# Kernel optimization log

Measured on AMD Instinct MI355X. Metric: run time of the kernel, lower is better.

The kernel has to match this reference:

```python
import jax, jax.numpy as jnp
import numpy as np

DIM = 512
HEADS = 8
HD = DIM // HEADS

def _rotate_half(t):
    t1, t2 = jnp.split(t, 2, axis=-1)
    return jnp.concatenate((-t2, t1), axis=-1)

def _layernorm(x, g, b, eps=1e-5):
    mu = jnp.mean(x, axis=-1, keepdims=True)
    var = jnp.var(x, axis=-1, keepdims=True)
    return (x - mu) * jax.lax.rsqrt(var + eps) * g + b

def setup_inputs() -> dict:
    key = jax.random.key(0)
    ks = jax.random.split(key, 12)
    B, S = 4, 2048
    x = jax.random.normal(ks[0], (B, S, DIM), dtype=jnp.float32)
    rope_cos = jax.random.uniform(ks[1], (1, S, 1, HD), dtype=jnp.float32)
    rope_sin = jax.random.uniform(ks[2], (1, S, 1, HD), dtype=jnp.float32)
    sd = 1.0 / np.sqrt(DIM)
    params = {
        'norm1_g': jnp.ones((DIM,), jnp.float32),
        'norm1_b': jnp.zeros((DIM,), jnp.float32),
        'norm2_g': jnp.ones((DIM,), jnp.float32),
        'norm2_b': jnp.zeros((DIM,), jnp.float32),
        'w_qkv': jax.random.uniform(ks[3], (DIM, 3 * DIM), jnp.float32, -sd, sd),
        'b_qkv': jax.random.uniform(ks[4], (3 * DIM,), jnp.float32, -sd, sd),
        'w_proj': jax.random.uniform(ks[5], (DIM, DIM), jnp.float32, -sd, sd),
        'b_proj': jax.random.uniform(ks[6], (DIM,), jnp.float32, -sd, sd),
        'w_fc1': jax.random.uniform(ks[7], (DIM, 4 * DIM), jnp.float32, -sd, sd),
        'b_fc1': jax.random.uniform(ks[8], (4 * DIM,), jnp.float32, -sd, sd),
        'w_fc2': jax.random.uniform(ks[9], (4 * DIM, DIM), jnp.float32, -1.0 / np.sqrt(4 * DIM), 1.0 / np.sqrt(4 * DIM)),
        'b_fc2': jax.random.uniform(ks[10], (DIM,), jnp.float32, -1.0 / np.sqrt(4 * DIM), 1.0 / np.sqrt(4 * DIM)),
    }
    return {'x': x, 'rope_cos': rope_cos, 'rope_sin': rope_sin, **params}

def reference(x, rope_cos, rope_sin, norm1_g, norm1_b, norm2_g, norm2_b,
              w_qkv, b_qkv, w_proj, b_proj, w_fc1, b_fc1, w_fc2, b_fc2):
    B, S, D = x.shape
    scale = 1.0 / np.sqrt(HD)
    shortcut = x
    h = _layernorm(x, norm1_g, norm1_b)
    qkv = (h @ w_qkv + b_qkv).reshape(B, S, 3, HEADS, HD)
    q, k, v = qkv[:, :, 0], qkv[:, :, 1], qkv[:, :, 2]  # [B,S,H,hd]
    q = q * rope_cos + _rotate_half(q) * rope_sin
    k = k * rope_cos + _rotate_half(k) * rope_sin
    # attention over heads: scores [B,H,S,S]
    attn = jnp.einsum('bqhd,bkhd->bhqk', q, k) * scale
    attn = jax.nn.softmax(attn, axis=-1)
    o = jnp.einsum('bhqk,bkhd->bqhd', attn, v).reshape(B, S, D)
    o = o @ w_proj + b_proj
    x = shortcut + o  # dropout is identity in eval
    h2 = _layernorm(x, norm2_g, norm2_b)
    mlp = jax.nn.gelu(h2 @ w_fc1 + b_fc1, approximate=False) @ w_fc2 + b_fc2
    return x + mlp
```

## Files before the change

### kernel.cpp

```cpp
#include <hip/hip_runtime.h>
#include <cstdint>
#include <cstddef>

typedef unsigned short u16;
typedef unsigned int   u32;
typedef __bf16 bf16x8 __attribute__((ext_vector_type(8)));
typedef float  f32x4  __attribute__((ext_vector_type(4)));

#define BS   8192
#define DIMM 512
#define NH   8
#define HD   64
#define SEQ  2048
#define DFF  2048
#define NQKV 1536

#define GLD16(g, l) __builtin_amdgcn_global_load_lds( \
    (__attribute__((address_space(1))) const void*)(g), \
    (__attribute__((address_space(3))) void*)(l), 16, 0, 0)

__device__ __forceinline__ float b2f(u16 s) {
  u32 u = ((u32)s) << 16;
  float f; __builtin_memcpy(&f, &u, 4); return f;
}
__device__ __forceinline__ u16 f2b(float f) {
  u32 u; __builtin_memcpy(&u, &f, 4);
  u += 0x7fffu + ((u >> 16) & 1u);
  return (u16)(u >> 16);
}
__device__ __forceinline__ u16 f2b_rtz(float f) {
  u32 u; __builtin_memcpy(&u, &f, 4);
  return (u16)(u >> 16);
}

#define SZ_QKV (DIMM * NQKV)
#define SZ_PRJ (DIMM * DIMM)
#define SZ_F1  (DIMM * DFF)
#define SZ_F2  (DFF * DIMM)
__global__ __launch_bounds__(256) void transpose_all_k(
    const float* __restrict__ w_qkv, const float* __restrict__ w_prj,
    const float* __restrict__ w_f1,  const float* __restrict__ w_f2,
    u16* __restrict__ o_qkv, u16* __restrict__ o_prj,
    u16* __restrict__ o_f1,  u16* __restrict__ o_f2) {
  int idx = blockIdx.x * 256 + threadIdx.x;
  const float* W; u16* O; int Kd, Nd, off;
  if (idx < SZ_QKV)                         { W = w_qkv; O = o_qkv; Kd = DIMM; Nd = NQKV; off = idx; }
  else if (idx < SZ_QKV + SZ_PRJ)           { W = w_prj; O = o_prj; Kd = DIMM; Nd = DIMM; off = idx - SZ_QKV; }
  else if (idx < SZ_QKV + SZ_PRJ + SZ_F1)   { W = w_f1;  O = o_f1;  Kd = DIMM; Nd = DFF;  off = idx - SZ_QKV - SZ_PRJ; }
  else                                      { W = w_f2;  O = o_f2;  Kd = DFF;  Nd = DIMM; off = idx - SZ_QKV - SZ_PRJ - SZ_F1; }
  int n = off / Kd, k = off - n * Kd;
  O[off] = f2b(W[(size_t)k * Nd + n]);
}

__global__ __launch_bounds__(256) void ln_f32b_k(const float* __restrict__ X,
    const float* __restrict__ G, const float* __restrict__ Bb, u16* __restrict__ out) {
  int w = threadIdx.x >> 6, lane = threadIdx.x & 63;
  size_t row = (size_t)blockIdx.x * 4 + w;
  const float* xr = X + row * DIMM;
  float v[8];
  *(float4*)&v[0] = *(const float4*)(xr + lane * 8);
  *(float4*)&v[4] = *(const float4*)(xr + lane * 8 + 4);
  float s = 0.f, s2 = 0.f;
#pragma unroll
  for (int j = 0; j < 8; j++) { s += v[j]; s2 += v[j] * v[j]; }
#pragma unroll
  for (int m = 1; m < 64; m <<= 1) { s += __shfl_xor(s, m); s2 += __shfl_xor(s2, m); }
  float mu = s * (1.f / DIMM);
  float rsd = rsqrtf(s2 * (1.f / DIMM) - mu * mu + 1e-5f);
  float g[8], bb[8];
  *(float4*)&g[0]  = *(const float4*)(G + lane * 8);
  *(float4*)&g[4]  = *(const float4*)(G + lane * 8 + 4);
  *(float4*)&bb[0] = *(const float4*)(Bb + lane * 8);
  *(float4*)&bb[4] = *(const float4*)(Bb + lane * 8 + 4);
  uint4 ov; u16* os = (u16*)&ov;
#pragma unroll
  for (int j = 0; j < 8; j++) os[j] = f2b((v[j] - mu) * rsd * g[j] + bb[j]);
  *(uint4*)(out + row * DIMM + lane * 8) = ov;
}

template <int EPI, int TM>
__global__ __launch_bounds__(256) void gemm_bt(const u16* __restrict__ A,
    const u16* __restrict__ BT, const float* __restrict__ bias,
    void* __restrict__ Cout, const float* __restrict__ resid, int N, int Kd) {
  __shared__ u16 a_s[TM * 32];
  __shared__ u16 b_s[128 * 32];
  int t = threadIdx.x, lane = t & 63, w = t >> 6;
  int l15 = lane & 15, quad = lane >> 4;
  int gx = gridDim.x;
  int lid = blockIdx.x + gx * blockIdx.y;
  int per = (gx * gridDim.y) >> 3;
  int nid = (lid & 7) * per + (lid >> 3);
  int bx = nid % gx, by = nid / gx;
  int m0 = by * TM, n0 = bx * 128;
  constexpr int MT = TM / 32;
  int wm = (w >> 1) * (TM / 2), wn = (w & 1) * 64;
  f32x4 z4 = {0.f, 0.f, 0.f, 0.f};
  f32x4 acc[MT][4];
#pragma unroll
  for (int i = 0; i < MT; i++)
#pragma unroll
    for (int j = 0; j < 4; j++) acc[i][j] = z4;

  for (int k0 = 0; k0 < Kd; k0 += 32) {
    __syncthreads();
#pragma unroll
    for (int i = 0; i < TM / 64; i++) {
      int c = t + i * 256;
      int row = c >> 2, ch = c & 3;
      GLD16(A + (size_t)(m0 + row) * Kd + k0 + ch * 8, &a_s[c * 8]);
    }
#pragma unroll
    for (int i = 0; i < 2; i++) {
      int c = t + i * 256;
      int row = c >> 2, ch = c & 3;
      GLD16(BT + (size_t)(n0 + row) * Kd + k0 + ch * 8, &b_s[c * 8]);
    }
    __syncthreads();
    bf16x8 af[MT], bfm[4];
#pragma unroll
    for (int mt = 0; mt < MT; mt++) af[mt] = *(const bf16x8*)&a_s[(wm + mt * 16 + l15) * 32 + quad * 8];
#pragma unroll
    for (int nt = 0; nt < 4; nt++) bfm[nt] = *(const bf16x8*)&b_s[(wn + nt * 16 + l15) * 32 + quad * 8];
#pragma unroll
    for (int mt = 0; mt < MT; mt++)
#pragma unroll
      for (int nt = 0; nt < 4; nt++)
        acc[mt][nt] = __builtin_amdgcn_mfma_f32_16x16x32_bf16(af[mt], bfm[nt], acc[mt][nt], 0, 0, 0);
  }

#pragma unroll
  for (int nt = 0; nt < 4; nt++) {
    int col = n0 + wn + nt * 16 + l15;
    float bv = bias[col];
#pragma unroll
    for (int mt = 0; mt < MT; mt++) {
#pragma unroll
      for (int r = 0; r < 4; r++) {
        int rw = m0 + wm + mt * 16 + quad * 4 + r;
        float v = acc[mt][nt][r] + bv;
        size_t off = (size_t)rw * N + col;
        if (EPI == 0) {
          ((float*)Cout)[off] = v;
        } else if (EPI == 1) {
          ((float*)Cout)[off] = v + resid[off];
        } else if (EPI == 2) {
          ((u16*)Cout)[off] = f2b(0.5f * v * (1.f + erff(v * 0.70710678118654752f)));
        } else {
          ((u16*)Cout)[off] = f2b(v);
        }
      }
    }
  }
}

#define QSCALE 0.18033688f
__global__ __launch_bounds__(256) void rope_k(const u16* __restrict__ qkv,
    const float* __restrict__ C, const float* __restrict__ Sn,
    u16* __restrict__ Qo, u16* __restrict__ Ko, u16* __restrict__ Vo) {
  int idx = blockIdx.x * 256 + threadIdx.x;
  int row = idx / 192;
  int cn = idx - row * 192;
  int n0 = cn * 8;
  int comp = n0 >> 9;
  int hh = (n0 >> 6) & 7;
  int d0 = n0 & 63;
  int b = row >> 11, s = row & 2047;
  const u16* src = qkv + (size_t)row * NQKV;
  uint4 val = *(const uint4*)(src + n0);
  u16* vs = (u16*)&val;
  size_t oo = ((size_t)((b << 3) + hh) * SEQ + s) * HD + d0;
  if (comp == 2) { *(uint4*)(Vo + oo) = val; return; }
  uint4 pv = *(const uint4*)(src + (n0 ^ 32));
  u16* ps = (u16*)&pv;
  float cv[8], sv[8];
  *(float4*)&cv[0] = *(const float4*)(C + s * HD + d0);
  *(float4*)&cv[4] = *(const float4*)(C + s * HD + d0 + 4);
  *(float4*)&sv[0] = *(const float4*)(Sn + s * HD + d0);
  *(float4*)&sv[4] = *(const float4*)(Sn + s * HD + d0 + 4);
  float sgn = (d0 & 32) ? 1.f : -1.f;
  float sc = (comp == 0) ? QSCALE : 1.f;
  uint4 ov; u16* os = (u16*)&ov;
#pragma unroll
  for (int j = 0; j < 8; j++)
    os[j] = f2b(sc * (b2f(vs[j]) * cv[j] + sgn * b2f(ps[j]) * sv[j]));
  *(uint4*)((comp == 0 ? Qo : Ko) + oo) = ov;
}

__global__ __launch_bounds__(512) void attn_flash_k(const u16* __restrict__ Qg,
    const u16* __restrict__ Kg, const u16* __restrict__ Vg, u16* __restrict__ Og) {
  __shared__ u16 q_s[128 * 72];
  __shared__ u16 k_s[64 * 72];
  __shared__ u16 vt_s[64 * 72];
  int t = threadIdx.x, lane = t & 63, w = t >> 6;
  int l15 = lane & 15, quad = lane >> 4;
  int lid = blockIdx.x;
  int nid = (lid & 7) * 64 + (lid >> 3);
  int bh = nid >> 4;
  int qt0 = (nid & 15) * 128;
  int b = bh >> 3, h = bh & 7;
  const u16* Qp = Qg + (size_t)bh * SEQ * HD;
  const u16* Kp = Kg + (size_t)bh * SEQ * HD;
  const u16* Vp = Vg + (size_t)bh * SEQ * HD;
  int row = t >> 3, ch = t & 7;
  int r8 = row >> 3, r0 = row & 7;

#pragma unroll
  for (int i = 0; i < 2; i++) {
    int c = t + i * 512, qr = c >> 3, qc = c & 7;
    *(uint4*)&q_s[qr * 72 + qc * 8] = *(const uint4*)(Qp + (size_t)(qt0 + qr) * HD + qc * 8);
  }
  uint4 kr = *(const uint4*)(Kp + (size_t)row * HD + ch * 8);
  uint4 vr = *(const uint4*)(Vp + (size_t)row * HD + ch * 8);
  __syncthreads();
  bf16x8 qa[2];
  qa[0] = *(const bf16x8*)&q_s[(w * 16 + l15) * 72 + quad * 8];
  qa[1] = *(const bf16x8*)&q_s[(w * 16 + l15) * 72 + 32 + quad * 8];
  u16* p_s = q_s;
  f32x4 z4 = {0.f, 0.f, 0.f, 0.f};
  f32x4 of[4];
#pragma unroll
  for (int n = 0; n < 4; n++) of[n] = z4;
  float lrun[4] = {};

  for (int kt = 0; kt < SEQ; kt += 64) {
    __syncthreads();
    *(uint4*)&k_s[row * 72 + ch * 8] = kr;
    {
      u16* v0 = (u16*)&vr;
#pragma unroll
      for (int j = 0; j < 8; j++) {
        int d = ch * 8 + j;
        vt_s[d * 72 + ((r8 ^ ch) << 3) + r0] = v0[j];
      }
    }
    __syncthreads();
    if (kt + 64 < SEQ) {
      kr = *(const uint4*)(Kp + (size_t)(kt + 64 + row) * HD + ch * 8);
      vr = *(const uint4*)(Vp + (size_t)(kt + 64 + row) * HD + ch * 8);
    }
    f32x4 sf[4];
#pragma unroll
    for (int n = 0; n < 4; n++) sf[n] = z4;
    __builtin_amdgcn_s_setprio(1);
#pragma unroll
    for (int kk = 0; kk < 2; kk++)
#pragma unroll
      for (int n = 0; n < 4; n++) {
        bf16x8 kb = *(const bf16x8*)&k_s[(n * 16 + l15) * 72 + kk * 32 + quad * 8];
        sf[n] = __builtin_amdgcn_mfma_f32_16x16x32_bf16(qa[kk], kb, sf[n], 0, 0, 0);
      }
    __builtin_amdgcn_s_setprio(0);
#pragma unroll
    for (int r = 0; r < 4; r++) {
      int prow = (w * 16 + quad * 4 + r) * 72;
#pragma unroll
      for (int n = 0; n < 4; n++) {
        float pp = exp2f(sf[n][r]);
        lrun[r] += pp;
        p_s[prow + n * 16 + l15] = f2b_rtz(pp);
      }
    }
    __builtin_amdgcn_s_setprio(1);
#pragma unroll
    for (int kk = 0; kk < 2; kk++) {
      bf16x8 pa = *(const bf16x8*)&p_s[(w * 16 + l15) * 72 + kk * 32 + quad * 8];
#pragma unroll
      for (int n = 0; n < 4; n++) {
        bf16x8 vb = *(const bf16x8*)&vt_s[(n * 16 + l15) * 72 +
                     (((kk * 4 + quad) ^ (2 * n + (l15 >> 3))) << 3)];
        of[n] = __builtin_amdgcn_mfma_f32_16x16x32_bf16(pa, vb, of[n], 0, 0, 0);
      }
    }
    __builtin_amdgcn_s_setprio(0);
  }
#pragma unroll
  for (int r = 0; r < 4; r++) {
    float l = lrun[r];
#pragma unroll
    for (int m = 1; m < 16; m <<= 1) l += __shfl_xor(l, m);
    float inv = 1.f / l;
    size_t orow = (size_t)(b * SEQ + qt0 + w * 16 + quad * 4 + r);
#pragma unroll
    for (int n = 0; n < 4; n++)
      Og[orow * DIMM + h * HD + n * 16 + l15] = f2b(of[n][r] * inv);
  }
}

extern "C" void kernel_launch(void* const* d_in, const int* in_sizes, int n_in,
                              void* d_out, int out_size, void* d_ws, size_t ws_size,
                              hipStream_t stream) {
  const float* x    = (const float*)d_in[0];
  const float* rc   = (const float*)d_in[1];
  const float* rsn  = (const float*)d_in[2];
  const float* n1g  = (const float*)d_in[3];
  const float* n1b  = (const float*)d_in[4];
  const float* n2g  = (const float*)d_in[5];
  const float* n2b  = (const float*)d_in[6];
  const float* wqkv = (const float*)d_in[7];
  const float* bqkv = (const float*)d_in[8];
  const float* wprj = (const float*)d_in[9];
  const float* bprj = (const float*)d_in[10];
  const float* wf1  = (const float*)d_in[11];
  const float* bf1  = (const float*)d_in[12];
  const float* wf2  = (const float*)d_in[13];
  const float* bf2  = (const float*)d_in[14];

  char* p = (char*)d_ws;
  u16*   wqkvT = (u16*)p;
  u16*   wprjT = (u16*)(p + (2u  << 20));
  u16*   wf1T  = (u16*)(p + (3u  << 20));
  u16*   wf2T  = (u16*)(p + (5u  << 20));
  u16*   h1    = (u16*)(p + (8u  << 20));
  u16*   qkvb  = (u16*)(p + (16u << 20));
  u16*   Qb    = (u16*)(p + (64u << 20));
  u16*   Kb    = (u16*)(p + (72u << 20));
  u16*   Vb    = (u16*)(p + (80u << 20));
  float* x2    = (float*)(p + (88u << 20));
  u16*   ob    = h1;
  u16*   h2    = h1;
  u16*   mid   = qkvb;

  transpose_all_k<<<dim3((SZ_QKV + SZ_PRJ + SZ_F1 + SZ_F2) / 256), 256, 0, stream>>>(
      wqkv, wprj, wf1, wf2, wqkvT, wprjT, wf1T, wf2T);

  ln_f32b_k<<<dim3(BS / 4), 256, 0, stream>>>(x, n1g, n1b, h1);

  gemm_bt<3, 128><<<dim3(NQKV / 128, BS / 128), 256, 0, stream>>>(h1, wqkvT, bqkv, qkvb, nullptr, NQKV, DIMM);

  rope_k<<<dim3(BS * NQKV / 8 / 256), 256, 0, stream>>>(qkvb, rc, rsn, Qb, Kb, Vb);

  attn_flash_k<<<dim3(32 * (SEQ / 128)), 512, 0, stream>>>(Qb, Kb, Vb, ob);

  gemm_bt<1, 64><<<dim3(DIMM / 128, BS / 64), 256, 0, stream>>>(ob, wprjT, bprj, x2, x, DIMM, DIMM);

  ln_f32b_k<<<dim3(BS / 4), 256, 0, stream>>>(x2, n2g, n2b, h2);

  gemm_bt<2, 128><<<dim3(DFF / 128, BS / 128), 256, 0, stream>>>(h2, wf1T, bf1, mid, nullptr, DFF, DIMM);

  gemm_bt<1, 64><<<dim3(DIMM / 128, BS / 64), 256, 0, stream>>>(mid, wf2T, bf2, (float*)d_out, x2, DIMM, DFF);
}
```

Measured before the change: 312.5 us.

## Double-buffer GEMM LDS tiles with XOR swizzle and retile N=512 GEMMs

The GEMM kernel now uses two LDS buffers, so the async global-to-LDS loads for the next K step are issued while MFMAs run on the current one. This halves the barriers per K step. LDS chunks are XOR-swizzled to cut bank conflicts on fragment reads. The projection and FC2 GEMMs move to 64x64 tiles with BK=64, where each wave owns a 16-row strip, which doubles block count for those narrow-N launches. The cost is double the LDS use, and the loop assumes an even number of K steps.

```diff
diff --git a/kernel.cpp b/kernel.cpp
--- a/kernel.cpp
+++ b/kernel.cpp
@@ -78,12 +78,20 @@
   *(uint4*)(out + row * DIMM + lane * 8) = ov;
 }
 
-template <int EPI, int TM>
+template <int EPI, int TM, int TN, int BK>
 __global__ __launch_bounds__(256) void gemm_bt(const u16* __restrict__ A,
     const u16* __restrict__ BT, const float* __restrict__ bias,
     void* __restrict__ Cout, const float* __restrict__ resid, int N, int Kd) {
-  __shared__ u16 a_s[TM * 32];
-  __shared__ u16 b_s[128 * 32];
+  constexpr int CPR  = BK / 8;
+  constexpr int CPRB = (BK == 64) ? 3 : 2;
+  constexpr int RS   = (BK == 64) ? 0 : 1;
+  constexpr int KK   = BK / 32;
+  constexpr int WROWS = (TN == 128) ? TM / 2 : TM / 4;
+  constexpr int MT   = WROWS / 16;
+  constexpr int ALOOP = TM * CPR / 256;
+  constexpr int BLOOP = TN * CPR / 256;
+  __shared__ __align__(16) u16 a_s[2][TM * BK];
+  __shared__ __align__(16) u16 b_s[2][TN * BK];
   int t = threadIdx.x, lane = t & 63, w = t >> 6;
   int l15 = lane & 15, quad = lane >> 4;
   int gx = gridDim.x;
@@ -91,9 +99,9 @@
   int per = (gx * gridDim.y) >> 3;
   int nid = (lid & 7) * per + (lid >> 3);
   int bx = nid % gx, by = nid / gx;
-  int m0 = by * TM, n0 = bx * 128;
-  constexpr int MT = TM / 32;
-  int wm = (w >> 1) * (TM / 2), wn = (w & 1) * 64;
+  int m0 = by * TM, n0 = bx * TN;
+  int wm = (TN == 128) ? (w >> 1) * WROWS : w * WROWS;
+  int wn = (TN == 128) ? (w & 1) * 64 : 0;
   f32x4 z4 = {0.f, 0.f, 0.f, 0.f};
   f32x4 acc[MT][4];
 #pragma unroll
@@ -101,32 +109,67 @@
 #pragma unroll
     for (int j = 0; j < 4; j++) acc[i][j] = z4;
 
-  for (int k0 = 0; k0 < Kd; k0 += 32) {
+#define GSTAGE(buf, ts) do {                                                  \
+    int k0_ = (ts) * BK;                                                      \
+    _Pragma("unroll")                                                         \
+    for (int i = 0; i < ALOOP; i++) {                                         \
+      int c_ = t + i * 256;                                                   \
+      int row_ = c_ >> CPRB, pos_ = c_ & (CPR - 1);                           \
+      int ch_ = (pos_ ^ (row_ >> RS)) & (CPR - 1);                            \
+      GLD16(A + (size_t)(m0 + row_) * Kd + k0_ + ch_ * 8, &a_s[buf][c_ * 8]); \
+    }                                                                         \
+    _Pragma("unroll")                                                         \
+    for (int i = 0; i < BLOOP; i++) {                                         \
+      int c_ = t + i * 256;                                                   \
+      int row_ = c_ >> CPRB, pos_ = c_ & (CPR - 1);                           \
+      int ch_ = (pos_ ^ (row_ >> RS)) & (CPR - 1);                            \
+      GLD16(BT + (size_t)(n0 + row_) * Kd + k0_ + ch_ * 8, &b_s[buf][c_ * 8]);\
+    }                                                                         \
+  } while (0)
+
+#define GCOMPUTE(buf) do {                                                    \
+    bf16x8 af[MT][KK], bfm[4][KK];                                            \
+    _Pragma("unroll")                                                         \
+    for (int mt = 0; mt < MT; mt++) {                                         \
+      _Pragma("unroll")                                                       \
+      for (int kk = 0; kk < KK; kk++) {                                       \
+        int row_ = wm + mt * 16 + l15;                                        \
+        int pos_ = ((kk * 4 + quad) ^ (row_ >> RS)) & (CPR - 1);              \
+        af[mt][kk] = *(const bf16x8*)&a_s[buf][row_ * BK + pos_ * 8];         \
+      }                                                                       \
+    }                                                                         \
+    _Pragma("unroll")                                                         \
+    for (int nt = 0; nt < 4; nt++) {                                          \
+      _Pragma("unroll")                                                       \
+      for (int kk = 0; kk < KK; kk++) {                                       \
+        int row_ = wn + nt * 16 + l15;                                        \
+        int pos_ = ((kk * 4 + quad) ^ (row_ >> RS)) & (CPR - 1);              \
+        bfm[nt][kk] = *(const bf16x8*)&b_s[buf][row_ * BK + pos_ * 8];        \
+      }                                                                       \
+    }                                                                         \
+    _Pragma("unroll")                                                         \
+    for (int kk = 0; kk < KK; kk++)                                           \
+      _Pragma("unroll")                                                       \
+      for (int mt = 0; mt < MT; mt++)                                         \
+        _Pragma("unroll")                                                     \
+        for (int nt = 0; nt < 4; nt++)                                        \
+          acc[mt][nt] = __builtin_amdgcn_mfma_f32_16x16x32_bf16(              \
+              af[mt][kk], bfm[nt][kk], acc[mt][nt], 0, 0, 0);                 \
+  } while (0)
+
+  GSTAGE(0, 0);
+  __syncthreads();
+  int nsteps = Kd / BK;
+  for (int ts = 0; ts < nsteps; ts += 2) {
+    GSTAGE(1, ts + 1);
+    GCOMPUTE(0);
     __syncthreads();
-#pragma unroll
-    for (int i = 0; i < TM / 64; i++) {
-      int c = t + i * 256;
-      int row = c >> 2, ch = c & 3;
-      GLD16(A + (size_t)(m0 + row) * Kd + k0 + ch * 8, &a_s[c * 8]);
-    }
-#pragma unroll
-    for (int i = 0; i < 2; i++) {
-      int c = t + i * 256;
-      int row = c >> 2, ch = c & 3;
-      GLD16(BT + (size_t)(n0 + row) * Kd + k0 + ch * 8, &b_s[c * 8]);
-    }
+    if (ts + 2 < nsteps) GSTAGE(0, ts + 2);
+    GCOMPUTE(1);
     __syncthreads();
-    bf16x8 af[MT], bfm[4];
-#pragma unroll
-    for (int mt = 0; mt < MT; mt++) af[mt] = *(const bf16x8*)&a_s[(wm + mt * 16 + l15) * 32 + quad * 8];
-#pragma unroll
-    for (int nt = 0; nt < 4; nt++) bfm[nt] = *(const bf16x8*)&b_s[(wn + nt * 16 + l15) * 32 + quad * 8];
-#pragma unroll
-    for (int mt = 0; mt < MT; mt++)
-#pragma unroll
-      for (int nt = 0; nt < 4; nt++)
-        acc[mt][nt] = __builtin_amdgcn_mfma_f32_16x16x32_bf16(af[mt], bfm[nt], acc[mt][nt], 0, 0, 0);
-  }
+  }
+#undef GSTAGE
+#undef GCOMPUTE
 
 #pragma unroll
   for (int nt = 0; nt < 4; nt++) {
@@ -325,17 +368,17 @@
 
   ln_f32b_k<<<dim3(BS / 4), 256, 0, stream>>>(x, n1g, n1b, h1);
 
-  gemm_bt<3, 128><<<dim3(NQKV / 128, BS / 128), 256, 0, stream>>>(h1, wqkvT, bqkv, qkvb, nullptr, NQKV, DIMM);
+  gemm_bt<3, 128, 128, 32><<<dim3(NQKV / 128, BS / 128), 256, 0, stream>>>(h1, wqkvT, bqkv, qkvb, nullptr, NQKV, DIMM);
 
   rope_k<<<dim3(BS * NQKV / 8 / 256), 256, 0, stream>>>(qkvb, rc, rsn, Qb, Kb, Vb);
 
   attn_flash_k<<<dim3(32 * (SEQ / 128)), 512, 0, stream>>>(Qb, Kb, Vb, ob);
 
-  gemm_bt<1, 64><<<dim3(DIMM / 128, BS / 64), 256, 0, stream>>>(ob, wprjT, bprj, x2, x, DIMM, DIMM);
+  gemm_bt<1, 64, 64, 64><<<dim3(DIMM / 64, BS / 64), 256, 0, stream>>>(ob, wprjT, bprj, x2, x, DIMM, DIMM);
 
   ln_f32b_k<<<dim3(BS / 4), 256, 0, stream>>>(x2, n2g, n2b, h2);
 
-  gemm_bt<2, 128><<<dim3(DFF / 128, BS / 128), 256, 0, stream>>>(h2, wf1T, bf1, mid, nullptr, DFF, DIMM);
-
-  gemm_bt<1, 64><<<dim3(DIMM / 128, BS / 64), 256, 0, stream>>>(mid, wf2T, bf2, (float*)d_out, x2, DIMM, DFF);
-}
+  gemm_bt<2, 128, 128, 32><<<dim3(DFF / 128, BS / 128), 256, 0, stream>>>(h2, wf1T, bf1, mid, nullptr, DFF, DIMM);
+
+  gemm_bt<1, 64, 64, 64><<<dim3(DIMM / 64, BS / 64), 256, 0, stream>>>(mid, wf2T, bf2, (float*)d_out, x2, DIMM, DFF);
+}
```

After: 305.4 us. 2.3% less time.
